# Performance work log

Hardware: AMD Instinct MI355X
Metric: run time of the kernel (lower is better)

## Reference

```python
import jax, jax.numpy as jnp
import numpy as np
import math

B, N, H, HEADS = 2, 4096, 256, 4
DH = H // HEADS
SCALE = math.sqrt(DH)


def setup_inputs() -> dict:
    key = jax.random.key(0)
    ks = jax.random.split(key, 8)
    h = jax.random.normal(ks[0], (B, N, H), dtype=jnp.float32)
    tau = jax.random.uniform(ks[1], (B, N), dtype=jnp.float32)  # trust scores in [0,1]
    adj_mask = jax.random.randint(ks[2], (N, N), 0, 2, dtype=jnp.int32)
    s = 0.02
    Wq = jax.random.normal(ks[3], (H, H), dtype=jnp.float32) * s
    Wk = jax.random.normal(ks[4], (H, H), dtype=jnp.float32) * s
    Wv = jax.random.normal(ks[5], (H, H), dtype=jnp.float32) * s
    Wo = jax.random.normal(ks[6], (H, H), dtype=jnp.float32) * s
    cw = jax.random.normal(ks[7], (HEADS,), dtype=jnp.float32) * s  # credibility_proj weight (num_heads,1) squeezed
    bq = jnp.zeros((H,), jnp.float32)
    bk = jnp.zeros((H,), jnp.float32)
    bv = jnp.zeros((H,), jnp.float32)
    bo = jnp.zeros((H,), jnp.float32)
    cb = jnp.zeros((HEADS,), jnp.float32)
    return {"h": h, "tau": tau, "adj_mask": adj_mask,
            "Wq": Wq, "bq": bq, "Wk": Wk, "bk": bk, "Wv": Wv, "bv": bv,
            "cw": cw, "cb": cb, "Wo": Wo, "bo": bo}


def reference(h, tau, adj_mask, Wq, bq, Wk, bk, Wv, bv, cw, cb, Wo, bo):
    # QKV projections -> (B, heads, N, head_dim)
    def proj(x, W, b):
        y = jnp.einsum('bnh,oh->bno', x, W) + b
        return y.reshape(B, N, HEADS, DH).transpose(0, 2, 1, 3)

    Q = proj(h, Wq, bq)
    K = proj(h, Wk, bk)
    V = proj(h, Wv, bv)

    scores = jnp.einsum('bhnd,bhmd->bhnm', Q, K) / SCALE  # (B,heads,N,N)
    # credibility bias: Linear(1 -> heads) applied to tau_i * tau_j
    tt = tau[:, :, None] * tau[:, None, :]                 # (B,N,N)
    cred = tt[:, None, :, :] * cw[None, :, None, None] + cb[None, :, None, None]
    scores = scores + cred
    # adjacency mask
    scores = jnp.where(adj_mask[None, None, :, :] == 0, -jnp.inf, scores)
    attention = jax.nn.softmax(scores, axis=-1)
    # dropout is identity in eval mode
    h_out = jnp.einsum('bhnm,bhmd->bhnd', attention, V)
    h_out = h_out.transpose(0, 2, 1, 3).reshape(B, N, H)
    h_out = jnp.einsum('bnh,oh->bno', h_out, Wo) + bo
    return h_out, attention.mean(axis=1)
```

## Files before the change

### kernel.cpp

```cpp
#include <hip/hip_runtime.h>

#define B_ 2
#define N_ 4096
#define H_ 256
#define HEADS_ 4
#define DH_ 64

typedef _Float16 f16;
typedef f16 f16x8 __attribute__((ext_vector_type(8)));
typedef f16 f16x4 __attribute__((ext_vector_type(4)));
typedef float f32x4 __attribute__((ext_vector_type(4)));


#define HOUT_OFF 2097152

__global__ __launch_bounds__(256) void cvt_kernel(
    const float* __restrict__ h, const float* __restrict__ Wq,
    const float* __restrict__ Wk, const float* __restrict__ Wv,
    const float* __restrict__ Wo, f16* __restrict__ ws) {
  int i = blockIdx.x * 256 + threadIdx.x;
  const int NH = 2097152;
  if (i < NH) {
    ws[i] = (f16)h[i];
  } else if (i < NH + 4 * 65536) {
    int j = i - NH;
    int sel = j >> 16;
    int k = j & 65535;
    const float* src = sel == 0 ? Wq : sel == 1 ? Wk : sel == 2 ? Wv : Wo;
    ws[i] = (f16)src[k];
  }
}

__global__ __launch_bounds__(256) void pack_adj_kernel(
    const int* __restrict__ adj, unsigned long long* __restrict__ adjb) {
  int g = blockIdx.x * 256 + threadIdx.x;
  int lane = threadIdx.x & 63;
  int av = adj[g] != 0;
  unsigned long long m = __ballot(av);
  if (lane == 0) adjb[g >> 6] = m;
}

__global__ __launch_bounds__(256) void proj_kernel(
    const f16* __restrict__ hh, const f16* __restrict__ Wh,
    const float* __restrict__ bq, const float* __restrict__ bk,
    const float* __restrict__ bv, f16* __restrict__ Qh, f16* __restrict__ Kf,
    f16* __restrict__ Vf) {
  const int tid = threadIdx.x;
  const int lane = tid & 63, w = tid >> 6;
  const int q = lane >> 4, c = lane & 15;
  const int wsel = blockIdx.y >> 2, head = blockIdx.y & 3;
  const int m0 = blockIdx.x * 64 + w * 16;
  const f16* W = Wh + wsel * 65536;
  const int o0 = head * 64;

  f32x4 acc[4] = {};
  for (int k0 = 0; k0 < 256; k0 += 32) {
    f16x8 a = *(const f16x8*)(hh + (size_t)(m0 + c) * 256 + k0 + q * 8);
#pragma unroll
    for (int cg = 0; cg < 4; ++cg) {
      f16x8 bfr = *(const f16x8*)(W + (size_t)(o0 + cg * 16 + c) * 256 + k0 + q * 8);
      acc[cg] = __builtin_amdgcn_mfma_f32_16x16x32_f16(a, bfr, acc[cg], 0, 0, 0);
    }
  }
  const int b = m0 >> 12, n = m0 & 4095;
  const int bh2 = b * HEADS_ + head;
  if (wsel == 2) {
    const int jt = n >> 6;
    f16* vbase = Vf + (((size_t)bh2 * 64 + jt) * 8) * 512;
#pragma unroll
    for (int cg = 0; cg < 4; ++cg) {
      float bb = bv[o0 + cg * 16 + c];
#pragma unroll
      for (int r = 0; r < 4; ++r) {
        int jj = w * 16 + q * 4 + r;
        vbase[(size_t)(((jj >> 5) * 4 + cg) * 512) + ((jj >> 3) & 3) * 128 +
              c * 8 + (jj & 7)] = (f16)(acc[cg][r] + bb);
      }
    }
  } else if (wsel == 1) {
    const int t = n >> 4;
    f16* kbase = Kf + (((size_t)bh2 * 256 + t) * 2) * 512;
#pragma unroll
    for (int cg = 0; cg < 4; ++cg) {
      float bb = bk[o0 + cg * 16 + c];
      const int half = cg >> 1;
      const int qf = ((cg & 1) * 16 + c) >> 3;
      f16* kb2 = kbase + half * 512 + qf * 128 + (c & 7);
#pragma unroll
      for (int r = 0; r < 4; ++r) kb2[(q * 4 + r) * 8] = (f16)(acc[cg][r] + bb);
    }
  } else {
#pragma unroll
    for (int cg = 0; cg < 4; ++cg) {
      int dh = cg * 16 + c;
      float bb = bq[o0 + dh];
#pragma unroll
      for (int r = 0; r < 4; ++r)
        Qh[((size_t)bh2 * N_ + n + q * 4 + r) * DH_ + dh] =
            (f16)((acc[cg][r] + bb) * 0.125f);
    }
  }
}

#define TS 68
#define WTILE (16 * TS)

__global__ __launch_bounds__(256) void attn_sum_kernel(
    const f16* __restrict__ Qh, const f16* __restrict__ Kf,
    const f16* __restrict__ Vf, const float* __restrict__ tau,
    const uint2* __restrict__ adjb, const float* __restrict__ cw,
    f16* __restrict__ Oh, float* __restrict__ rsum_ws) {
  __shared__ float lds[4 * WTILE];
  __shared__ float lred[4][16];
  const int gid = blockIdx.x;
  const int bh = gid & 7;
  const int b = bh >> 2, h = bh & 3;
  const int i0 = (gid >> 3) * 16;
  const int tid = threadIdx.x;
  const int lane = tid & 63, jq = tid >> 6;
  const int q = lane >> 4, c = lane & 15;

  const f16* Qbase = Qh + ((size_t)bh * N_ + i0 + c) * DH_;
  f16x8 a0 = *(const f16x8*)(Qbase + q * 8);
  f16x8 a1 = *(const f16x8*)(Qbase + 32 + q * 8);

  const float cw_h = cw[h];
  float tau_i[4];
#pragma unroll
  for (int r = 0; r < 4; ++r) tau_i[r] = tau[b * N_ + i0 + q * 4 + r];
  const f16* Kfb = Kf + (size_t)bh * 262144 + lane * 8;
  const f16* Vfb = Vf + (size_t)bh * 262144 + lane * 8;
  const float* taub = tau + b * N_;
  const int jbase = jq * 1024;

  float lsum[4] = {0.f, 0.f, 0.f, 0.f};
  f32x4 oacc[4] = {};
  float* myp = lds + jq * WTILE;

  f16x8 kf[2][8];
  f16x8 vf[8];
  {
    const f16* kt = Kfb + (size_t)(jbase >> 4) * 1024;
#pragma unroll
    for (int f = 0; f < 8; ++f) kf[0][f] = *(const f16x8*)(kt + f * 512);
  }

#pragma unroll 2
  for (int it = 0; it < 16; ++it) {
    const int cur = it & 1, nx = cur ^ 1;
    const int j0 = jbase + it * 64;
    const int jn = j0 + (it < 15 ? 64 : 0);
    uint2 aw[4];
    float tj[4];
#pragma unroll
    for (int r = 0; r < 4; ++r)
      aw[r] = adjb[(size_t)(i0 + q * 4 + r) * 64 + (j0 >> 6)];
#pragma unroll
    for (int cg = 0; cg < 4; ++cg) tj[cg] = taub[j0 + cg * 16 + c];
    {
      const f16* vt = Vfb + (size_t)(j0 >> 6) * 4096;
#pragma unroll
      for (int f = 0; f < 8; ++f) vf[f] = *(const f16x8*)(vt + f * 512);
    }

#pragma unroll
    for (int cg = 0; cg < 4; ++cg) {
      f32x4 s = {};
      s = __builtin_amdgcn_mfma_f32_16x16x32_f16(a0, kf[cur][2 * cg], s, 0, 0, 0);
      s = __builtin_amdgcn_mfma_f32_16x16x32_f16(a1, kf[cur][2 * cg + 1], s, 0, 0, 0);
      const float credj = cw_h * tj[cg];
      const unsigned shift = (cg & 1) * 16 + c;
#pragma unroll
      for (int r = 0; r < 4; ++r) {
        unsigned mword = (cg < 2) ? aw[r].x : aw[r].y;
        float e = __expf(s[r] + credj * tau_i[r]);
        e = ((mword >> shift) & 1) ? e : 0.f;
        lsum[r] += e;
        myp[(q * 4 + r) * TS + cg * 16 + c] = e;
      }
    }
    {
      const f16* kt = Kfb + (size_t)(jn >> 4) * 1024;
#pragma unroll
      for (int f = 0; f < 8; ++f) kf[nx][f] = *(const f16x8*)(kt + f * 512);
    }
#pragma unroll
    for (int ks = 0; ks < 2; ++ks) {
      f32x4 plo = *(f32x4*)(myp + c * TS + ks * 32 + q * 8);
      f32x4 phi = *(f32x4*)(myp + c * TS + ks * 32 + q * 8 + 4);
      f16x8 pa;
#pragma unroll
      for (int t = 0; t < 4; ++t) {
        pa[t] = (f16)plo[t];
        pa[4 + t] = (f16)phi[t];
      }
#pragma unroll
      for (int cg = 0; cg < 4; ++cg)
        oacc[cg] =
            __builtin_amdgcn_mfma_f32_16x16x32_f16(pa, vf[ks * 4 + cg], oacc[cg], 0, 0, 0);
    }
  }

#pragma unroll
  for (int r = 0; r < 4; ++r) {
    float v = lsum[r];
    v += __shfl_xor(v, 1);
    v += __shfl_xor(v, 2);
    v += __shfl_xor(v, 4);
    v += __shfl_xor(v, 8);
    lsum[r] = v;
  }
  if (c == 0) {
#pragma unroll
    for (int r = 0; r < 4; ++r) lred[jq][q * 4 + r] = lsum[r];
  }
  __syncthreads();
  float linv[4];
#pragma unroll
  for (int r = 0; r < 4; ++r)
    linv[r] = 1.0f / (lred[0][q * 4 + r] + lred[1][q * 4 + r] +
                      lred[2][q * 4 + r] + lred[3][q * 4 + r]);
  if (jq == 0 && c == 0) {
#pragma unroll
    for (int r = 0; r < 4; ++r) rsum_ws[bh * N_ + i0 + q * 4 + r] = linv[r];
  }

  if (jq != 0) {
#pragma unroll
    for (int cg = 0; cg < 4; ++cg)
#pragma unroll
      for (int r = 0; r < 4; ++r) myp[(cg * 4 + r) * 64 + lane] = oacc[cg][r];
  }
  __syncthreads();
  if (jq == 0) {
#pragma unroll
    for (int cg = 0; cg < 4; ++cg)
#pragma unroll
      for (int r = 0; r < 4; ++r) {
        float v = oacc[cg][r];
#pragma unroll
        for (int jj = 1; jj < 4; ++jj)
          v += lds[jj * WTILE + (cg * 4 + r) * 64 + lane];
        Oh[((size_t)(b * N_) + i0 + q * 4 + r) * H_ + h * 64 + cg * 16 + c] =
            (f16)(v * linv[r]);
      }
  }
}

__global__ __launch_bounds__(256) void attn_mean_kernel(
    const f16* __restrict__ Qh, const f16* __restrict__ Kf,
    const float* __restrict__ tau, const uint2* __restrict__ adjb,
    const float* __restrict__ cw, const float* __restrict__ linv_ws,
    float* __restrict__ out) {
  const int gid = blockIdx.x;
  const int b = gid & 1;
  const int jq = (gid >> 1) & 3;
  const int i0 = (gid >> 3) * 16;
  const int tid = threadIdx.x;
  const int lane = tid & 63, w = tid >> 6;
  const int q = lane >> 4, c = lane & 15;

  f16x8 a0[4], a1[4];
  float li[4][4];
  float cwh[4];
#pragma unroll
  for (int h = 0; h < 4; ++h) {
    const f16* Qbase = Qh + ((size_t)(b * 4 + h) * N_ + i0 + c) * DH_;
    a0[h] = *(const f16x8*)(Qbase + q * 8);
    a1[h] = *(const f16x8*)(Qbase + 32 + q * 8);
    cwh[h] = cw[h];
#pragma unroll
    for (int r = 0; r < 4; ++r)
      li[h][r] = linv_ws[(b * 4 + h) * N_ + i0 + q * 4 + r] * 0.25f;
  }
  float tau_i[4];
#pragma unroll
  for (int r = 0; r < 4; ++r) tau_i[r] = tau[b * N_ + i0 + q * 4 + r];
  const float* taub = tau + b * N_;

  for (int it = 0; it < 4; ++it) {
    const int j0 = jq * 1024 + (it * 4 + w) * 64;
    uint2 aw[4];
#pragma unroll
    for (int r = 0; r < 4; ++r)
      aw[r] = adjb[(size_t)(i0 + q * 4 + r) * 64 + (j0 >> 6)];
    float tj[4];
#pragma unroll
    for (int cg = 0; cg < 4; ++cg) tj[cg] = taub[j0 + cg * 16 + c];

    const f16* KfT = Kf + (size_t)(b * 4) * 262144 + (size_t)(j0 >> 4) * 1024 +
                     lane * 8;
    f16x8 kf2[2][8];
#pragma unroll
    for (int f = 0; f < 8; ++f) kf2[0][f] = *(const f16x8*)(KfT + f * 512);

    f32x4 macc[4] = {};
#pragma unroll
    for (int h = 0; h < 4; ++h) {
      const int cur = h & 1, nx = cur ^ 1;
      if (h < 3) {
        const f16* Kn = KfT + (size_t)(h + 1) * 262144;
#pragma unroll
        for (int f = 0; f < 8; ++f) kf2[nx][f] = *(const f16x8*)(Kn + f * 512);
      }
#pragma unroll
      for (int cg = 0; cg < 4; ++cg) {
        f32x4 s = {};
        s = __builtin_amdgcn_mfma_f32_16x16x32_f16(a0[h], kf2[cur][2 * cg], s, 0, 0, 0);
        s = __builtin_amdgcn_mfma_f32_16x16x32_f16(a1[h], kf2[cur][2 * cg + 1], s, 0, 0, 0);
        const float credj = cwh[h] * tj[cg];
        const unsigned shift = (cg & 1) * 16 + c;
#pragma unroll
        for (int r = 0; r < 4; ++r) {
          unsigned mword = (cg < 2) ? aw[r].x : aw[r].y;
          float e = __expf(s[r] + credj * tau_i[r]);
          float lw = ((mword >> shift) & 1) ? li[h][r] : 0.f;
          macc[cg][r] += e * lw;
        }
      }
    }
#pragma unroll
    for (int cg = 0; cg < 4; ++cg)
#pragma unroll
      for (int r = 0; r < 4; ++r)
        out[((size_t)(b * N_) + i0 + q * 4 + r) * N_ + j0 + cg * 16 + c] =
            macc[cg][r];
  }
}

__global__ __launch_bounds__(256) void oproj_kernel(
    const f16* __restrict__ Oh, const f16* __restrict__ Woh,
    const float* __restrict__ bo, float* __restrict__ out) {
  const int tid = threadIdx.x, lane = tid & 63, w = tid >> 6;
  const int q = lane >> 4, c = lane & 15;
  const int m0 = blockIdx.x * 64 + w * 16;
  const int o0 = blockIdx.y * 64;
  f32x4 acc[4] = {};
  for (int k0 = 0; k0 < 256; k0 += 32) {
    f16x8 a = *(const f16x8*)(Oh + (size_t)(m0 + c) * 256 + k0 + q * 8);
#pragma unroll
    for (int cg = 0; cg < 4; ++cg) {
      f16x8 bfr = *(const f16x8*)(Woh + (size_t)(o0 + cg * 16 + c) * 256 + k0 + q * 8);
      acc[cg] = __builtin_amdgcn_mfma_f32_16x16x32_f16(a, bfr, acc[cg], 0, 0, 0);
    }
  }
#pragma unroll
  for (int cg = 0; cg < 4; ++cg) {
    float bb = bo[o0 + cg * 16 + c];
#pragma unroll
    for (int r = 0; r < 4; ++r)
      out[(size_t)(m0 + q * 4 + r) * 256 + o0 + cg * 16 + c] = acc[cg][r] + bb;
  }
}

extern "C" void kernel_launch(void* const* d_in, const int* in_sizes, int n_in,
                              void* d_out, int out_size, void* d_ws,
                              size_t ws_size, hipStream_t stream) {
  const float* h   = (const float*)d_in[0];
  const float* tau = (const float*)d_in[1];
  const int*   adj = (const int*)d_in[2];
  const float* Wq  = (const float*)d_in[3];
  const float* bq  = (const float*)d_in[4];
  const float* Wk  = (const float*)d_in[5];
  const float* bk  = (const float*)d_in[6];
  const float* Wv  = (const float*)d_in[7];
  const float* bv  = (const float*)d_in[8];
  const float* cw  = (const float*)d_in[9];
  const float* Wo  = (const float*)d_in[11];
  const float* bo  = (const float*)d_in[12];
  float* out = (float*)d_out;

  f16* ws   = (f16*)d_ws;
  f16* h_h  = ws;
  f16* W_h  = ws + 2097152;
  f16* Wo_h = W_h + 3 * 65536;
  f16* Q_h  = ws + 2359296;
  f16* K_f  = ws + 4456448;
  f16* V_f  = ws + 6553600;
  f16* O_h  = ws + 8650752;
  unsigned long long* adjb = (unsigned long long*)(ws + 10747904);
  float* rsum_ws = (float*)ws;

  pack_adj_kernel<<<dim3(65536), dim3(256), 0, stream>>>(adj, adjb);
  cvt_kernel<<<dim3(9216), dim3(256), 0, stream>>>(h, Wq, Wk, Wv, Wo, ws);
  proj_kernel<<<dim3(128, 12), dim3(256), 0, stream>>>(h_h, W_h, bq, bk, bv, Q_h,
                                                       K_f, V_f);
  attn_sum_kernel<<<dim3(2048), dim3(256), 0, stream>>>(
      Q_h, K_f, V_f, tau, (const uint2*)adjb, cw, O_h, rsum_ws);
  attn_mean_kernel<<<dim3(2048), dim3(256), 0, stream>>>(
      Q_h, K_f, tau, (const uint2*)adjb, cw, rsum_ws, out + HOUT_OFF);
  oproj_kernel<<<dim3(128, 4), dim3(256), 0, stream>>>(O_h, Wo_h, bo, out);
}
```

Baseline: 427.5 us.

## Process multiple query row-groups per block to reuse K/V tiles

attn_sum now handles 64 query rows per block (four 16-row groups), and attn_mean handles 32 rows. Each K/V tile loaded from global memory is reused across those groups, which cuts K/V reload traffic and shrinks the grids from 2048 to 512 and 1024 blocks. The cost is higher register pressure (more accumulators, hence launch_bounds min 2), loss of the old K double-buffer prefetch, and fewer blocks to hide latency. The output reduction now runs per group with extra syncthreads.

```diff
diff --git a/kernel.cpp b/kernel.cpp
--- a/kernel.cpp
+++ b/kernel.cpp
@@ -105,149 +105,163 @@
 #define TS 68
 #define WTILE (16 * TS)
 
-__global__ __launch_bounds__(256) void attn_sum_kernel(
+__global__ __launch_bounds__(256, 2) void attn_sum_kernel(
     const f16* __restrict__ Qh, const f16* __restrict__ Kf,
     const f16* __restrict__ Vf, const float* __restrict__ tau,
     const uint2* __restrict__ adjb, const float* __restrict__ cw,
     f16* __restrict__ Oh, float* __restrict__ rsum_ws) {
   __shared__ float lds[4 * WTILE];
-  __shared__ float lred[4][16];
+  __shared__ float lred[4][64];
   const int gid = blockIdx.x;
   const int bh = gid & 7;
   const int b = bh >> 2, h = bh & 3;
-  const int i0 = (gid >> 3) * 16;
+  const int i0 = (gid >> 3) * 64;
   const int tid = threadIdx.x;
   const int lane = tid & 63, jq = tid >> 6;
   const int q = lane >> 4, c = lane & 15;
 
-  const f16* Qbase = Qh + ((size_t)bh * N_ + i0 + c) * DH_;
-  f16x8 a0 = *(const f16x8*)(Qbase + q * 8);
-  f16x8 a1 = *(const f16x8*)(Qbase + 32 + q * 8);
-
+  f16x8 a0[4], a1[4];
+  float tau_i[4][4];
+#pragma unroll
+  for (int ig = 0; ig < 4; ++ig) {
+    const f16* Qbase = Qh + ((size_t)bh * N_ + i0 + ig * 16 + c) * DH_;
+    a0[ig] = *(const f16x8*)(Qbase + q * 8);
+    a1[ig] = *(const f16x8*)(Qbase + 32 + q * 8);
+#pragma unroll
+    for (int r = 0; r < 4; ++r)
+      tau_i[ig][r] = tau[b * N_ + i0 + ig * 16 + q * 4 + r];
+  }
   const float cw_h = cw[h];
-  float tau_i[4];
-#pragma unroll
-  for (int r = 0; r < 4; ++r) tau_i[r] = tau[b * N_ + i0 + q * 4 + r];
   const f16* Kfb = Kf + (size_t)bh * 262144 + lane * 8;
   const f16* Vfb = Vf + (size_t)bh * 262144 + lane * 8;
   const float* taub = tau + b * N_;
   const int jbase = jq * 1024;
 
-  float lsum[4] = {0.f, 0.f, 0.f, 0.f};
-  f32x4 oacc[4] = {};
+  float lsum[4][4] = {};
+  f32x4 oacc[4][4] = {};
   float* myp = lds + jq * WTILE;
 
-  f16x8 kf[2][8];
-  f16x8 vf[8];
-  {
-    const f16* kt = Kfb + (size_t)(jbase >> 4) * 1024;
-#pragma unroll
-    for (int f = 0; f < 8; ++f) kf[0][f] = *(const f16x8*)(kt + f * 512);
-  }
-
-#pragma unroll 2
+#pragma unroll 1
   for (int it = 0; it < 16; ++it) {
-    const int cur = it & 1, nx = cur ^ 1;
     const int j0 = jbase + it * 64;
-    const int jn = j0 + (it < 15 ? 64 : 0);
-    uint2 aw[4];
-    float tj[4];
-#pragma unroll
-    for (int r = 0; r < 4; ++r)
-      aw[r] = adjb[(size_t)(i0 + q * 4 + r) * 64 + (j0 >> 6)];
-#pragma unroll
-    for (int cg = 0; cg < 4; ++cg) tj[cg] = taub[j0 + cg * 16 + c];
+    f16x8 kf[8], vf[8];
+    {
+      const f16* kt = Kfb + (size_t)(j0 >> 4) * 1024;
+#pragma unroll
+      for (int f = 0; f < 8; ++f) kf[f] = *(const f16x8*)(kt + f * 512);
+    }
     {
       const f16* vt = Vfb + (size_t)(j0 >> 6) * 4096;
 #pragma unroll
       for (int f = 0; f < 8; ++f) vf[f] = *(const f16x8*)(vt + f * 512);
     }
-
-#pragma unroll
-    for (int cg = 0; cg < 4; ++cg) {
-      f32x4 s = {};
-      s = __builtin_amdgcn_mfma_f32_16x16x32_f16(a0, kf[cur][2 * cg], s, 0, 0, 0);
-      s = __builtin_amdgcn_mfma_f32_16x16x32_f16(a1, kf[cur][2 * cg + 1], s, 0, 0, 0);
-      const float credj = cw_h * tj[cg];
-      const unsigned shift = (cg & 1) * 16 + c;
-#pragma unroll
-      for (int r = 0; r < 4; ++r) {
-        unsigned mword = (cg < 2) ? aw[r].x : aw[r].y;
-        float e = __expf(s[r] + credj * tau_i[r]);
-        e = ((mword >> shift) & 1) ? e : 0.f;
-        lsum[r] += e;
-        myp[(q * 4 + r) * TS + cg * 16 + c] = e;
+    float tj[4];
+#pragma unroll
+    for (int cg = 0; cg < 4; ++cg) tj[cg] = taub[j0 + cg * 16 + c];
+
+#pragma unroll
+    for (int ig = 0; ig < 4; ++ig) {
+      uint2 aw[4];
+#pragma unroll
+      for (int r = 0; r < 4; ++r)
+        aw[r] = adjb[(size_t)(i0 + ig * 16 + q * 4 + r) * 64 + (j0 >> 6)];
+#pragma unroll
+      for (int cg = 0; cg < 4; ++cg) {
+        f32x4 s = {};
+        s = __builtin_amdgcn_mfma_f32_16x16x32_f16(a0[ig], kf[2 * cg], s, 0, 0, 0);
+        s = __builtin_amdgcn_mfma_f32_16x16x32_f16(a1[ig], kf[2 * cg + 1], s, 0, 0, 0);
+        const float credj = cw_h * tj[cg];
+        const unsigned shift = (cg & 1) * 16 + c;
+#pragma unroll
+        for (int r = 0; r < 4; ++r) {
+          unsigned mword = (cg < 2) ? aw[r].x : aw[r].y;
+          float e = __expf(s[r] + credj * tau_i[ig][r]);
+          e = ((mword >> shift) & 1) ? e : 0.f;
+          lsum[ig][r] += e;
+          myp[(q * 4 + r) * TS + cg * 16 + c] = e;
+        }
       }
-    }
-    {
-      const f16* kt = Kfb + (size_t)(jn >> 4) * 1024;
-#pragma unroll
-      for (int f = 0; f < 8; ++f) kf[nx][f] = *(const f16x8*)(kt + f * 512);
-    }
-#pragma unroll
-    for (int ks = 0; ks < 2; ++ks) {
-      f32x4 plo = *(f32x4*)(myp + c * TS + ks * 32 + q * 8);
-      f32x4 phi = *(f32x4*)(myp + c * TS + ks * 32 + q * 8 + 4);
-      f16x8 pa;
-#pragma unroll
-      for (int t = 0; t < 4; ++t) {
-        pa[t] = (f16)plo[t];
-        pa[4 + t] = (f16)phi[t];
+#pragma unroll
+      for (int ks = 0; ks < 2; ++ks) {
+        f32x4 plo = *(f32x4*)(myp + c * TS + ks * 32 + q * 8);
+        f32x4 phi = *(f32x4*)(myp + c * TS + ks * 32 + q * 8 + 4);
+        f16x8 pa;
+#pragma unroll
+        for (int t = 0; t < 4; ++t) {
+          pa[t] = (f16)plo[t];
+          pa[4 + t] = (f16)phi[t];
+        }
+#pragma unroll
+        for (int cg = 0; cg < 4; ++cg)
+          oacc[ig][cg] = __builtin_amdgcn_mfma_f32_16x16x32_f16(
+              pa, vf[ks * 4 + cg], oacc[ig][cg], 0, 0, 0);
       }
+    }
+  }
+
+#pragma unroll
+  for (int ig = 0; ig < 4; ++ig) {
+#pragma unroll
+    for (int r = 0; r < 4; ++r) {
+      float v = lsum[ig][r];
+      v += __shfl_xor(v, 1);
+      v += __shfl_xor(v, 2);
+      v += __shfl_xor(v, 4);
+      v += __shfl_xor(v, 8);
+      lsum[ig][r] = v;
+    }
+  }
+  if (c == 0) {
+#pragma unroll
+    for (int ig = 0; ig < 4; ++ig)
+#pragma unroll
+      for (int r = 0; r < 4; ++r) lred[jq][ig * 16 + q * 4 + r] = lsum[ig][r];
+  }
+  __syncthreads();
+  float linv[4][4];
+#pragma unroll
+  for (int ig = 0; ig < 4; ++ig)
+#pragma unroll
+    for (int r = 0; r < 4; ++r) {
+      int row = ig * 16 + q * 4 + r;
+      linv[ig][r] = 1.0f / (lred[0][row] + lred[1][row] + lred[2][row] +
+                            lred[3][row]);
+    }
+  if (jq == 0 && c == 0) {
+#pragma unroll
+    for (int ig = 0; ig < 4; ++ig)
+#pragma unroll
+      for (int r = 0; r < 4; ++r)
+        rsum_ws[bh * N_ + i0 + ig * 16 + q * 4 + r] = linv[ig][r];
+  }
+
+#pragma unroll 1
+  for (int ig = 0; ig < 4; ++ig) {
+    if (jq != 0) {
 #pragma unroll
       for (int cg = 0; cg < 4; ++cg)
-        oacc[cg] =
-            __builtin_amdgcn_mfma_f32_16x16x32_f16(pa, vf[ks * 4 + cg], oacc[cg], 0, 0, 0);
-    }
-  }
-
-#pragma unroll
-  for (int r = 0; r < 4; ++r) {
-    float v = lsum[r];
-    v += __shfl_xor(v, 1);
-    v += __shfl_xor(v, 2);
-    v += __shfl_xor(v, 4);
-    v += __shfl_xor(v, 8);
-    lsum[r] = v;
-  }
-  if (c == 0) {
-#pragma unroll
-    for (int r = 0; r < 4; ++r) lred[jq][q * 4 + r] = lsum[r];
-  }
-  __syncthreads();
-  float linv[4];
-#pragma unroll
-  for (int r = 0; r < 4; ++r)
-    linv[r] = 1.0f / (lred[0][q * 4 + r] + lred[1][q * 4 + r] +
-                      lred[2][q * 4 + r] + lred[3][q * 4 + r]);
-  if (jq == 0 && c == 0) {
-#pragma unroll
-    for (int r = 0; r < 4; ++r) rsum_ws[bh * N_ + i0 + q * 4 + r] = linv[r];
-  }
-
-  if (jq != 0) {
-#pragma unroll
-    for (int cg = 0; cg < 4; ++cg)
-#pragma unroll
-      for (int r = 0; r < 4; ++r) myp[(cg * 4 + r) * 64 + lane] = oacc[cg][r];
-  }
-  __syncthreads();
-  if (jq == 0) {
-#pragma unroll
-    for (int cg = 0; cg < 4; ++cg)
-#pragma unroll
-      for (int r = 0; r < 4; ++r) {
-        float v = oacc[cg][r];
-#pragma unroll
-        for (int jj = 1; jj < 4; ++jj)
-          v += lds[jj * WTILE + (cg * 4 + r) * 64 + lane];
-        Oh[((size_t)(b * N_) + i0 + q * 4 + r) * H_ + h * 64 + cg * 16 + c] =
-            (f16)(v * linv[r]);
-      }
-  }
-}
-
-__global__ __launch_bounds__(256) void attn_mean_kernel(
+#pragma unroll
+        for (int r = 0; r < 4; ++r) myp[(cg * 4 + r) * 64 + lane] = oacc[ig][cg][r];
+    }
+    __syncthreads();
+    if (jq == 0) {
+#pragma unroll
+      for (int cg = 0; cg < 4; ++cg)
+#pragma unroll
+        for (int r = 0; r < 4; ++r) {
+          float v = oacc[ig][cg][r];
+#pragma unroll
+          for (int jj = 1; jj < 4; ++jj)
+            v += lds[jj * WTILE + (cg * 4 + r) * 64 + lane];
+          Oh[((size_t)(b * N_) + i0 + ig * 16 + q * 4 + r) * H_ + h * 64 +
+             cg * 16 + c] = (f16)(v * linv[ig][r]);
+        }
+    }
+    __syncthreads();
+  }
+}
+
+__global__ __launch_bounds__(256, 2) void attn_mean_kernel(
     const f16* __restrict__ Qh, const f16* __restrict__ Kf,
     const float* __restrict__ tau, const uint2* __restrict__ adjb,
     const float* __restrict__ cw, const float* __restrict__ linv_ws,
@@ -255,76 +269,85 @@
   const int gid = blockIdx.x;
   const int b = gid & 1;
   const int jq = (gid >> 1) & 3;
-  const int i0 = (gid >> 3) * 16;
+  const int i0 = (gid >> 3) * 32;
   const int tid = threadIdx.x;
   const int lane = tid & 63, w = tid >> 6;
   const int q = lane >> 4, c = lane & 15;
 
-  f16x8 a0[4], a1[4];
-  float li[4][4];
+  float li[4][2][4];
   float cwh[4];
 #pragma unroll
   for (int h = 0; h < 4; ++h) {
-    const f16* Qbase = Qh + ((size_t)(b * 4 + h) * N_ + i0 + c) * DH_;
-    a0[h] = *(const f16x8*)(Qbase + q * 8);
-    a1[h] = *(const f16x8*)(Qbase + 32 + q * 8);
     cwh[h] = cw[h];
 #pragma unroll
+    for (int ig = 0; ig < 2; ++ig)
+#pragma unroll
+      for (int r = 0; r < 4; ++r)
+        li[h][ig][r] =
+            linv_ws[(b * 4 + h) * N_ + i0 + ig * 16 + q * 4 + r] * 0.25f;
+  }
+  float tau_i[2][4];
+#pragma unroll
+  for (int ig = 0; ig < 2; ++ig)
+#pragma unroll
     for (int r = 0; r < 4; ++r)
-      li[h][r] = linv_ws[(b * 4 + h) * N_ + i0 + q * 4 + r] * 0.25f;
-  }
-  float tau_i[4];
-#pragma unroll
-  for (int r = 0; r < 4; ++r) tau_i[r] = tau[b * N_ + i0 + q * 4 + r];
+      tau_i[ig][r] = tau[b * N_ + i0 + ig * 16 + q * 4 + r];
   const float* taub = tau + b * N_;
 
+#pragma unroll 1
   for (int it = 0; it < 4; ++it) {
     const int j0 = jq * 1024 + (it * 4 + w) * 64;
-    uint2 aw[4];
-#pragma unroll
-    for (int r = 0; r < 4; ++r)
-      aw[r] = adjb[(size_t)(i0 + q * 4 + r) * 64 + (j0 >> 6)];
+    uint2 aw[2][4];
+#pragma unroll
+    for (int ig = 0; ig < 2; ++ig)
+#pragma unroll
+      for (int r = 0; r < 4; ++r)
+        aw[ig][r] = adjb[(size_t)(i0 + ig * 16 + q * 4 + r) * 64 + (j0 >> 6)];
     float tj[4];
 #pragma unroll
     for (int cg = 0; cg < 4; ++cg) tj[cg] = taub[j0 + cg * 16 + c];
 
-    const f16* KfT = Kf + (size_t)(b * 4) * 262144 + (size_t)(j0 >> 4) * 1024 +
-                     lane * 8;
-    f16x8 kf2[2][8];
-#pragma unroll
-    for (int f = 0; f < 8; ++f) kf2[0][f] = *(const f16x8*)(KfT + f * 512);
-
-    f32x4 macc[4] = {};
+    f32x4 macc[2][4] = {};
 #pragma unroll
     for (int h = 0; h < 4; ++h) {
-      const int cur = h & 1, nx = cur ^ 1;
-      if (h < 3) {
-        const f16* Kn = KfT + (size_t)(h + 1) * 262144;
-#pragma unroll
-        for (int f = 0; f < 8; ++f) kf2[nx][f] = *(const f16x8*)(Kn + f * 512);
+      f16x8 kf[8];
+      {
+        const f16* kt = Kf + (size_t)(b * 4 + h) * 262144 +
+                        (size_t)(j0 >> 4) * 1024 + lane * 8;
+#pragma unroll
+        for (int f = 0; f < 8; ++f) kf[f] = *(const f16x8*)(kt + f * 512);
       }
 #pragma unroll
-      for (int cg = 0; cg < 4; ++cg) {
-        f32x4 s = {};
-        s = __builtin_amdgcn_mfma_f32_16x16x32_f16(a0[h], kf2[cur][2 * cg], s, 0, 0, 0);
-        s = __builtin_amdgcn_mfma_f32_16x16x32_f16(a1[h], kf2[cur][2 * cg + 1], s, 0, 0, 0);
-        const float credj = cwh[h] * tj[cg];
-        const unsigned shift = (cg & 1) * 16 + c;
-#pragma unroll
-        for (int r = 0; r < 4; ++r) {
-          unsigned mword = (cg < 2) ? aw[r].x : aw[r].y;
-          float e = __expf(s[r] + credj * tau_i[r]);
-          float lw = ((mword >> shift) & 1) ? li[h][r] : 0.f;
-          macc[cg][r] += e * lw;
+      for (int ig = 0; ig < 2; ++ig) {
+        const f16* Qbase =
+            Qh + ((size_t)(b * 4 + h) * N_ + i0 + ig * 16 + c) * DH_;
+        f16x8 a0 = *(const f16x8*)(Qbase + q * 8);
+        f16x8 a1 = *(const f16x8*)(Qbase + 32 + q * 8);
+#pragma unroll
+        for (int cg = 0; cg < 4; ++cg) {
+          f32x4 s = {};
+          s = __builtin_amdgcn_mfma_f32_16x16x32_f16(a0, kf[2 * cg], s, 0, 0, 0);
+          s = __builtin_amdgcn_mfma_f32_16x16x32_f16(a1, kf[2 * cg + 1], s, 0, 0, 0);
+          const float credj = cwh[h] * tj[cg];
+          const unsigned shift = (cg & 1) * 16 + c;
+#pragma unroll
+          for (int r = 0; r < 4; ++r) {
+            unsigned mword = (cg < 2) ? aw[ig][r].x : aw[ig][r].y;
+            float e = __expf(s[r] + credj * tau_i[ig][r]);
+            float lw = ((mword >> shift) & 1) ? li[h][ig][r] : 0.f;
+            macc[ig][cg][r] += e * lw;
+          }
         }
       }
     }
 #pragma unroll
-    for (int cg = 0; cg < 4; ++cg)
-#pragma unroll
-      for (int r = 0; r < 4; ++r)
-        out[((size_t)(b * N_) + i0 + q * 4 + r) * N_ + j0 + cg * 16 + c] =
-            macc[cg][r];
+    for (int ig = 0; ig < 2; ++ig)
+#pragma unroll
+      for (int cg = 0; cg < 4; ++cg)
+#pragma unroll
+        for (int r = 0; r < 4; ++r)
+          out[((size_t)(b * N_) + i0 + ig * 16 + q * 4 + r) * N_ + j0 +
+              cg * 16 + c] = macc[ig][cg][r];
   }
 }
 
@@ -385,9 +408,9 @@
   cvt_kernel<<<dim3(9216), dim3(256), 0, stream>>>(h, Wq, Wk, Wv, Wo, ws);
   proj_kernel<<<dim3(128, 12), dim3(256), 0, stream>>>(h_h, W_h, bq, bk, bv, Q_h,
                                                        K_f, V_f);
-  attn_sum_kernel<<<dim3(2048), dim3(256), 0, stream>>>(
+  attn_sum_kernel<<<dim3(512), dim3(256), 0, stream>>>(
       Q_h, K_f, V_f, tau, (const uint2*)adjb, cw, O_h, rsum_ws);
-  attn_mean_kernel<<<dim3(2048), dim3(256), 0, stream>>>(
+  attn_mean_kernel<<<dim3(1024), dim3(256), 0, stream>>>(
       Q_h, K_f, tau, (const uint2*)adjb, cw, rsum_ws, out + HOUT_OFF);
   oproj_kernel<<<dim3(128, 4), dim3(256), 0, stream>>>(O_h, Wo_h, bo, out);
 }
```

Measured after the change: 392.0 us. -8.3%, faster.
